# Optimization experiments

Measured on AMD Instinct MI355X. Metric: run time of the kernel, lower is better.

Reference implementation:

```python
import jax, jax.numpy as jnp
import numpy as np
from jax import lax

CAP_UNITS = 49
CAP_SIZE = 8

def setup_inputs() -> dict:
    key = jax.random.key(0)
    k1, k2, k3 = jax.random.split(key, 3)
    x = jax.random.normal(k1, (128, 16, 64, 64), dtype=jnp.float32)
    # 49 ConvUnits (16->8, 9x9) stacked into one conv weight [49*8, 16, 9, 9]
    fan_in = 16 * 9 * 9
    bound = 1.0 / np.sqrt(fan_in)
    W = jax.random.uniform(k2, (CAP_UNITS * CAP_SIZE, 16, 9, 9), jnp.float32, -bound, bound)
    b = jax.random.uniform(k3, (CAP_UNITS * CAP_SIZE,), jnp.float32, -bound, bound)
    return {"x": x, "W": W, "b": b}

def squash(s, axis):
    mag_sq = jnp.sum(s * s, axis=axis, keepdims=True)
    mag = jnp.sqrt(mag_sq)
    return mag_sq / (1.0 + mag_sq) * (s / mag)

def reference(x, W, b):
    B = x.shape[0]
    # single fused conv == 49 parallel 16->8 convs, 9x9, stride 2, VALID
    h = lax.conv_general_dilated(
        x, W, window_strides=(2, 2), padding='VALID',
        dimension_numbers=('NCHW', 'OIHW', 'NCHW'))
    h = h + b[None, :, None, None]                    # [B, 49*8, H', W']
    Hp, Wp = h.shape[2], h.shape[3]
    u = h.reshape(B, CAP_UNITS, CAP_SIZE, Hp * Wp)    # [B, 49, 8, HW]
    # torch ordering: cat over units on dim 3 -> [B,8,HW,49] -> flatten -> capsule idx = hw*49 + unit
    u = u.transpose(0, 3, 1, 2).reshape(B, Hp * Wp * CAP_UNITS, CAP_SIZE)
    return squash(u, axis=2)
```

## Files before the change

### kernel.cpp

```cpp
#include <hip/hip_runtime.h>


typedef __attribute__((ext_vector_type(8)))  short short8;
typedef __attribute__((ext_vector_type(16))) float f32x16;

constexpr int Bn = 128, Units = 49, Cap = 8, OW = 28, HWp = 784;
constexpr int Nn = 392, Npad = 448;
constexpr int BM = 256, BNt = 64, NB = 7;
constexpr int NSLOT = 82;
constexpr size_t XW_BYTES = (size_t)Bn * 64 * 64 * 16 * 2;
constexpr size_t BW_BYTES = (size_t)NSLOT * 2 * Npad * 8 * 2;

__device__ inline unsigned short f2bf(float f) {
    unsigned u = __float_as_uint(f);
    u += 0x7FFF + ((u >> 16) & 1);
    return (unsigned short)(u >> 16);
}

__global__ __launch_bounds__(256) void prep_x(const float* __restrict__ x,
                                              unsigned short* __restrict__ xw) {
    __shared__ unsigned short tile[64 * 16];
    const int b = blockIdx.x >> 6, y = blockIdx.x & 63;
    const int t = threadIdx.x;
    const int c = t >> 4, x0 = (t & 15) * 4;
    const float4 v = *(const float4*)(x + (((size_t)b * 16 + c) * 64 + y) * 64 + x0);
    tile[(x0 + 0) * 16 + c] = f2bf(v.x);
    tile[(x0 + 1) * 16 + c] = f2bf(v.y);
    tile[(x0 + 2) * 16 + c] = f2bf(v.z);
    tile[(x0 + 3) * 16 + c] = f2bf(v.w);
    __syncthreads();
    const ushort4 o = *(const ushort4*)&tile[t * 4];
    *(ushort4*)(xw + (size_t)blockIdx.x * 1024 + t * 4) = o;
}

__global__ __launch_bounds__(256) void prep_w(const float* __restrict__ W,
                                              unsigned short* __restrict__ bw) {
    const int idx = blockIdx.x * 256 + threadIdx.x;
    if (idx >= NSLOT * 2 * Npad) return;
    const int n  = idx % Npad;
    const int ph = idx / Npad;
    const int h = ph & 1, p = ph >> 1;
    unsigned short vals[8];
    if (p < 81 && n < Nn) {
#pragma unroll
        for (int j = 0; j < 8; ++j)
            vals[j] = f2bf(W[(size_t)(n * 16 + h * 8 + j) * 81 + p]);
    } else {
#pragma unroll
        for (int j = 0; j < 8; ++j) vals[j] = 0;
    }
    *(ushort4*)(bw + (size_t)idx * 8)     = make_ushort4(vals[0], vals[1], vals[2], vals[3]);
    *(ushort4*)(bw + (size_t)idx * 8 + 4) = make_ushort4(vals[4], vals[5], vals[6], vals[7]);
}

#define MFMA32(A, B, C) __builtin_amdgcn_mfma_f32_32x32x16_bf16(A, B, C, 0, 0, 0)

__global__ __launch_bounds__(256, 3) void pcaps_mfma32(
    const unsigned short* __restrict__ xw,
    const unsigned short* __restrict__ bw,
    const float* __restrict__ bias,
    float* __restrict__ out)
{
    const int t = threadIdx.x;

    const int cpx  = gridDim.x >> 3;
    const int wgid = (blockIdx.x & 7) * cpx + (blockIdx.x >> 3);
    const int nb = wgid % NB, mb = wgid / NB;
    const int n0 = nb * BNt;

    const int w = t >> 6, l = t & 63;
    const int r = l & 31, h = l >> 5;

    int abase[2];
#pragma unroll
    for (int mi = 0; mi < 2; ++mi) {
        const int m = mb * BM + w * 64 + mi * 32 + r;
        const int b = m / HWp;
        const int hw = m - b * HWp;
        const int oy = hw / OW, ox = hw - oy * OW;
        abase[mi] = b * 131072 + oy * 4096 + ox * 64 + h * 16;
    }

    const char* __restrict__ a0 = (const char*)xw + abase[0];
    const char* __restrict__ a1 = (const char*)xw + abase[1];
    const char* __restrict__ bp = (const char*)bw + ((h * Npad) + n0 + r) * 16;

    f32x16 acc[2][2];
#pragma unroll
    for (int mi = 0; mi < 2; ++mi)
#pragma unroll
        for (int ni = 0; ni < 2; ++ni)
#pragma unroll
            for (int e = 0; e < 16; ++e) acc[mi][ni][e] = 0.f;

    short8 af[4][2], bf[4][2];
#pragma unroll
    for (int s = 0; s < 4; ++s) {
        const int off = (s / 9) * 2048 + (s % 9) * 32;
        af[s][0] = *(const short8*)(a0 + off);
        af[s][1] = *(const short8*)(a1 + off);
        bf[s][0] = *(const short8*)(bp + s * 14336);
        bf[s][1] = *(const short8*)(bp + s * 14336 + 512);
    }

#pragma unroll
    for (int s = 0; s < NSLOT; ++s) {
        const int p = s & 3;
        acc[0][0] = MFMA32(af[p][0], bf[p][0], acc[0][0]);
        acc[0][1] = MFMA32(af[p][0], bf[p][1], acc[0][1]);
        acc[1][0] = MFMA32(af[p][1], bf[p][0], acc[1][0]);
        acc[1][1] = MFMA32(af[p][1], bf[p][1], acc[1][1]);
        if (s + 4 < NSLOT) {
            const int s2  = s + 4;
            const int off = (s2 / 9) * 2048 + (s2 % 9) * 32;
            af[p][0] = *(const short8*)(a0 + off);
            af[p][1] = *(const short8*)(a1 + off);
            bf[p][0] = *(const short8*)(bp + s2 * 14336);
            bf[p][1] = *(const short8*)(bp + s2 * 14336 + 512);
        }
    }

    float bv[2];
#pragma unroll
    for (int ni = 0; ni < 2; ++ni) {
        const int n = n0 + ni * 32 + r;
        bv[ni] = (n < Nn) ? bias[n] : 0.f;
    }
#pragma unroll
    for (int mi = 0; mi < 2; ++mi) {
#pragma unroll
        for (int ni = 0; ni < 2; ++ni) {
            const int n = n0 + ni * 32 + r;
            const bool nok = (n < Nn);
#pragma unroll
            for (int reg = 0; reg < 16; ++reg) {
                float e = acc[mi][ni][reg] + bv[ni];
                float sq = e * e;
                sq += __shfl_xor(sq, 1);
                sq += __shfl_xor(sq, 2);
                sq += __shfl_xor(sq, 4);
                const float scale = sqrtf(sq) / (1.0f + sq);
                if (nok) {
                    const int rowc = (reg & 3) + 8 * (reg >> 2) + 4 * h;
                    const int m = mb * BM + w * 64 + mi * 32 + rowc;
                    out[(size_t)m * Nn + n] = e * scale;
                }
            }
        }
    }
}

__global__ __launch_bounds__(128) void pcaps_direct(
    const float* __restrict__ x, const float* __restrict__ W,
    const float* __restrict__ bias, float* __restrict__ out)
{
    const int blk = blockIdx.x;
    const int tile = blk % 7;
    const int u = (blk / 7) % Units;
    const int b = blk / (7 * Units);
    const int hw = tile * 128 + threadIdx.x;
    const bool active = (hw < HWp);
    const int oy = active ? (hw / OW) : 0;
    const int ox = active ? (hw % OW) : 0;
    const float* xb = x + (size_t)b * (16 * 64 * 64) + (size_t)(oy * 2) * 64 + ox * 2;
    const float* wu = W + (size_t)u * (Cap * 1296);
    float acc[Cap];
#pragma unroll
    for (int j = 0; j < Cap; ++j) acc[j] = bias[u * Cap + j];
    for (int c = 0; c < 16; ++c) {
        const float* xcp = xb + c * (64 * 64);
        const float* wc = wu + c * 81;
#pragma unroll
        for (int ky = 0; ky < 9; ++ky) {
            const float* xr = xcp + ky * 64;
            float xv[9];
#pragma unroll
            for (int kx = 0; kx < 9; ++kx) xv[kx] = xr[kx];
#pragma unroll
            for (int kx = 0; kx < 9; ++kx)
#pragma unroll
                for (int j = 0; j < Cap; ++j)
                    acc[j] = fmaf(xv[kx], wc[j * 1296 + ky * 9 + kx], acc[j]);
        }
    }
    if (active) {
        float msq = 0.f;
#pragma unroll
        for (int j = 0; j < Cap; ++j) msq = fmaf(acc[j], acc[j], msq);
        const float scale = sqrtf(msq) / (1.0f + msq);
        float* op = out + (size_t)b * (HWp * Nn) + (size_t)hw * Nn + u * Cap;
        float4 o0, o1;
        o0.x = acc[0] * scale; o0.y = acc[1] * scale; o0.z = acc[2] * scale; o0.w = acc[3] * scale;
        o1.x = acc[4] * scale; o1.y = acc[5] * scale; o1.z = acc[6] * scale; o1.w = acc[7] * scale;
        *reinterpret_cast<float4*>(op) = o0;
        *reinterpret_cast<float4*>(op + 4) = o1;
    }
}

extern "C" void kernel_launch(void* const* d_in, const int* in_sizes, int n_in,
                              void* d_out, int out_size, void* d_ws, size_t ws_size,
                              hipStream_t stream)
{
    const float* x  = (const float*)d_in[0];
    const float* W  = (const float*)d_in[1];
    const float* bs = (const float*)d_in[2];
    float* out      = (float*)d_out;

    if (ws_size < XW_BYTES + BW_BYTES) {
        pcaps_direct<<<Bn * Units * 7, 128, 0, stream>>>(x, W, bs, out);
        return;
    }

    unsigned short* xw = (unsigned short*)d_ws;
    unsigned short* bw = (unsigned short*)((char*)d_ws + XW_BYTES);

    prep_x<<<Bn * 64, 256, 0, stream>>>(x, xw);
    prep_w<<<(NSLOT * 2 * Npad + 255) / 256, 256, 0, stream>>>(W, bw);
    pcaps_mfma32<<<(100352 / BM) * NB, 256, 0, stream>>>(xw, bw, bs, out);
}
```

Before: 220.3 us.

## Stage A/B tiles through double-buffered LDS with async global_load_lds and larger M tile

Replaces the register-direct global-load MFMA loop with a double-buffered LDS pipeline. Async global_load_lds copies bring in swizzled im2col A rows and the B weights. The M tile doubles to 512, so each wave computes 4x2 32x32 tiles, and the K loop processes two tap slots per stage. The goal is to reuse loaded A and B fragments across more MFMAs and to overlap the next stage's loads with the current compute. In exchange it adds LDS use and a barrier every iteration, and lowers occupancy to 2 waves per SIMD.

Measured after the change: 220.7 us. About the same (+0.2%).

```diff
diff --git a/kernel.cpp b/kernel.cpp
--- a/kernel.cpp
+++ b/kernel.cpp
@@ -6,15 +6,21 @@
 
 constexpr int Bn = 128, Units = 49, Cap = 8, OW = 28, HWp = 784;
 constexpr int Nn = 392, Npad = 448;
-constexpr int BM = 256, BNt = 64, NB = 7;
-constexpr int NSLOT = 82;
+constexpr int BM = 512, BNt = 64, NB = 7;
+constexpr int NKS = 41;
 constexpr size_t XW_BYTES = (size_t)Bn * 64 * 64 * 16 * 2;
-constexpr size_t BW_BYTES = (size_t)NSLOT * 2 * Npad * 8 * 2;
+constexpr size_t BW_BYTES = (size_t)NKS * 4 * Npad * 8 * 2;
 
 __device__ inline unsigned short f2bf(float f) {
     unsigned u = __float_as_uint(f);
     u += 0x7FFF + ((u >> 16) & 1);
     return (unsigned short)(u >> 16);
+}
+
+__device__ __forceinline__ void gload16(const void* g, void* l) {
+    __builtin_amdgcn_global_load_lds(
+        (const __attribute__((address_space(1))) unsigned int*)g,
+        (__attribute__((address_space(3))) unsigned int*)l, 16, 0, 0);
 }
 
 __global__ __launch_bounds__(256) void prep_x(const float* __restrict__ x,
@@ -36,10 +42,11 @@
 __global__ __launch_bounds__(256) void prep_w(const float* __restrict__ W,
                                               unsigned short* __restrict__ bw) {
     const int idx = blockIdx.x * 256 + threadIdx.x;
-    if (idx >= NSLOT * 2 * Npad) return;
-    const int n  = idx % Npad;
-    const int ph = idx / Npad;
-    const int h = ph & 1, p = ph >> 1;
+    if (idx >= NKS * 4 * Npad) return;
+    const int n    = idx % Npad;
+    const int rest = idx / Npad;
+    const int h = rest & 1, tt = (rest >> 1) & 1, ks = rest >> 2;
+    const int p = ks * 2 + tt;
     unsigned short vals[8];
     if (p < 81 && n < Nn) {
 #pragma unroll
@@ -55,69 +62,118 @@
 
 #define MFMA32(A, B, C) __builtin_amdgcn_mfma_f32_32x32x16_bf16(A, B, C, 0, 0, 0)
 
-__global__ __launch_bounds__(256, 3) void pcaps_mfma32(
+constexpr int ABUF = 32768;
+constexpr int LBUF = ABUF + 4096;
+
+__global__ __launch_bounds__(256, 2) void pcaps_lds(
     const unsigned short* __restrict__ xw,
     const unsigned short* __restrict__ bw,
     const float* __restrict__ bias,
     float* __restrict__ out)
 {
+    __shared__ __align__(16) char lds[2][LBUF];
+
     const int t = threadIdx.x;
-
-    const int cpx  = gridDim.x >> 3;
-    const int wgid = (blockIdx.x & 7) * cpx + (blockIdx.x >> 3);
+    const int nwg = gridDim.x;
+    const int q8 = nwg >> 3, r8 = nwg & 7;
+    const int xcd = blockIdx.x & 7, idx8 = blockIdx.x >> 3;
+    const int wgid = (xcd < r8 ? xcd * (q8 + 1) : r8 * (q8 + 1) + (xcd - r8) * q8) + idx8;
     const int nb = wgid % NB, mb = wgid / NB;
     const int n0 = nb * BNt;
 
     const int w = t >> 6, l = t & 63;
     const int r = l & 31, h = l >> 5;
 
-    int abase[2];
-#pragma unroll
-    for (int mi = 0; mi < 2; ++mi) {
-        const int m = mb * BM + w * 64 + mi * 32 + r;
+    int arow_off[8];
+    int asel[8];
+#pragma unroll
+    for (int it = 0; it < 8; ++it) {
+        const int q = t + 256 * it;
+        const int row = q >> 2;
+        const int piece = (q & 3) ^ ((row >> 1) & 3);
+        const int tq = piece >> 1, hq = piece & 1;
+        const int m = mb * BM + row;
         const int b = m / HWp;
         const int hw = m - b * HWp;
         const int oy = hw / OW, ox = hw - oy * OW;
-        abase[mi] = b * 131072 + oy * 4096 + ox * 64 + h * 16;
-    }
-
-    const char* __restrict__ a0 = (const char*)xw + abase[0];
-    const char* __restrict__ a1 = (const char*)xw + abase[1];
-    const char* __restrict__ bp = (const char*)bw + ((h * Npad) + n0 + r) * 16;
-
-    f32x16 acc[2][2];
-#pragma unroll
-    for (int mi = 0; mi < 2; ++mi)
+        arow_off[it] = b * 131072 + oy * 4096 + ox * 64 + hq * 16;
+        asel[it] = tq;
+    }
+    const int bglob0 = (w * Npad + n0 + l) * 16;
+    constexpr int bstep = 4 * Npad * 16;
+
+    int aoff[4][2];
+#pragma unroll
+    for (int mi = 0; mi < 4; ++mi) {
+        const int row = w * 128 + mi * 32 + r;
+        const int cid0 = (row * 4 + h) ^ ((row >> 1) & 3);
+        aoff[mi][0] = cid0 * 16;
+        aoff[mi][1] = (cid0 ^ 2) * 16;
+    }
+    int boff[2][2];
+#pragma unroll
+    for (int ni = 0; ni < 2; ++ni)
+#pragma unroll
+        for (int tt = 0; tt < 2; ++tt)
+            boff[ni][tt] = ABUF + ((tt * 2 + h) * 64 + ni * 32 + r) * 16;
+
+    f32x16 acc[4][2];
+#pragma unroll
+    for (int mi = 0; mi < 4; ++mi)
 #pragma unroll
         for (int ni = 0; ni < 2; ++ni)
 #pragma unroll
             for (int e = 0; e < 16; ++e) acc[mi][ni][e] = 0.f;
 
-    short8 af[4][2], bf[4][2];
-#pragma unroll
-    for (int s = 0; s < 4; ++s) {
-        const int off = (s / 9) * 2048 + (s % 9) * 32;
-        af[s][0] = *(const short8*)(a0 + off);
-        af[s][1] = *(const short8*)(a1 + off);
-        bf[s][0] = *(const short8*)(bp + s * 14336);
-        bf[s][1] = *(const short8*)(bp + s * 14336 + 512);
-    }
-
-#pragma unroll
-    for (int s = 0; s < NSLOT; ++s) {
-        const int p = s & 3;
-        acc[0][0] = MFMA32(af[p][0], bf[p][0], acc[0][0]);
-        acc[0][1] = MFMA32(af[p][0], bf[p][1], acc[0][1]);
-        acc[1][0] = MFMA32(af[p][1], bf[p][0], acc[1][0]);
-        acc[1][1] = MFMA32(af[p][1], bf[p][1], acc[1][1]);
-        if (s + 4 < NSLOT) {
-            const int s2  = s + 4;
-            const int off = (s2 / 9) * 2048 + (s2 % 9) * 32;
-            af[p][0] = *(const short8*)(a0 + off);
-            af[p][1] = *(const short8*)(a1 + off);
-            bf[p][0] = *(const short8*)(bp + s2 * 14336);
-            bf[p][1] = *(const short8*)(bp + s2 * 14336 + 512);
+    const char* __restrict__ xcc = (const char*)xw;
+    const char* __restrict__ bcc = (const char*)bw;
+
+    auto stage = [&](char* base, int o0, int o1, int bks) {
+#pragma unroll
+        for (int it = 0; it < 8; ++it)
+            gload16(xcc + (arow_off[it] + (asel[it] ? o1 : o0)),
+                    base + (t + 256 * it) * 16);
+        gload16(bcc + (bglob0 + bks), base + ABUF + t * 16);
+    };
+
+    stage(lds[0], 0, 32, 0);
+    __syncthreads();
+
+    int ky = 0, kx = 2;
+    int cur = 0;
+    for (int ks = 0; ks < NKS; ++ks) {
+        if (ks + 1 < NKS) {
+            const int o0 = ky * 2048 + kx * 32;
+            int kx1 = kx + 1, ky1 = ky;
+            if (kx1 == 9) { kx1 = 0; ky1 += 1; }
+            const int o1 = ky1 * 2048 + kx1 * 32;
+            stage(lds[cur ^ 1], o0, o1, (ks + 1) * bstep);
+            kx += 2; if (kx >= 9) { kx -= 9; ky += 1; }
         }
+
+        const char* base = lds[cur];
+        short8 afr[4][2], bfr[2][2];
+#pragma unroll
+        for (int mi = 0; mi < 4; ++mi)
+#pragma unroll
+            for (int tt = 0; tt < 2; ++tt)
+                afr[mi][tt] = *(const short8*)(base + aoff[mi][tt]);
+#pragma unroll
+        for (int ni = 0; ni < 2; ++ni)
+#pragma unroll
+            for (int tt = 0; tt < 2; ++tt)
+                bfr[ni][tt] = *(const short8*)(base + boff[ni][tt]);
+
+#pragma unroll
+        for (int tt = 0; tt < 2; ++tt)
+#pragma unroll
+            for (int mi = 0; mi < 4; ++mi)
+#pragma unroll
+                for (int ni = 0; ni < 2; ++ni)
+                    acc[mi][ni] = MFMA32(afr[mi][tt], bfr[ni][tt], acc[mi][ni]);
+
+        __syncthreads();
+        cur ^= 1;
     }
 
     float bv[2];
@@ -127,7 +183,7 @@
         bv[ni] = (n < Nn) ? bias[n] : 0.f;
     }
 #pragma unroll
-    for (int mi = 0; mi < 2; ++mi) {
+    for (int mi = 0; mi < 4; ++mi) {
 #pragma unroll
         for (int ni = 0; ni < 2; ++ni) {
             const int n = n0 + ni * 32 + r;
@@ -142,7 +198,7 @@
                 const float scale = sqrtf(sq) / (1.0f + sq);
                 if (nok) {
                     const int rowc = (reg & 3) + 8 * (reg >> 2) + 4 * h;
-                    const int m = mb * BM + w * 64 + mi * 32 + rowc;
+                    const int m = mb * BM + w * 128 + mi * 32 + rowc;
                     out[(size_t)m * Nn + n] = e * scale;
                 }
             }
@@ -215,6 +271,6 @@
     unsigned short* bw = (unsigned short*)((char*)d_ws + XW_BYTES);
 
     prep_x<<<Bn * 64, 256, 0, stream>>>(x, xw);
-    prep_w<<<(NSLOT * 2 * Npad + 255) / 256, 256, 0, stream>>>(W, bw);
-    pcaps_mfma32<<<(100352 / BM) * NB, 256, 0, stream>>>(xw, bw, bs, out);
-}
+    prep_w<<<(NKS * 4 * Npad + 255) / 256, 256, 0, stream>>>(W, bw);
+    pcaps_lds<<<(100352 / BM) * NB, 256, 0, stream>>>(xw, bw, bs, out);
+}
```
